# Performance work log

Hardware: AMD Instinct MI355X
Metric: run time of the kernel (lower is better)

Reference implementation:

```python
import jax, jax.numpy as jnp
import numpy as np

H = 16        # heads
DH = 64       # dim_head
DM = 1024     # query_dim = context_dim
INNER = H * DH


def setup_inputs() -> dict:
    key = jax.random.key(0)
    ks = jax.random.split(key, 5)
    s = 0.02
    queries = jax.random.normal(ks[0], (2, 2048, DM), dtype=jnp.float32)
    Wq = jax.random.normal(ks[1], (DM, INNER), dtype=jnp.float32) * s
    Wkv = jax.random.normal(ks[2], (DM, 2 * INNER), dtype=jnp.float32) * s
    Wo = jax.random.normal(ks[3], (INNER, DM), dtype=jnp.float32) * s
    bo = jax.random.normal(ks[4], (DM,), dtype=jnp.float32) * s
    return {"queries": queries, "Wq": Wq, "Wkv": Wkv, "Wo": Wo, "bo": bo}


def reference(queries, Wq, Wkv, Wo, bo):
    b, n, _ = queries.shape
    scale = DH ** -0.5
    q = queries @ Wq                       # [b, n, inner]
    kv = queries @ Wkv                     # self-attention: context = queries
    k, v = jnp.split(kv, 2, axis=-1)
    # b n (h d) -> b h n d
    split_heads = lambda t: t.reshape(b, n, H, DH).transpose(0, 2, 1, 3)
    q, k, v = map(split_heads, (q, k, v))
    sim = jnp.einsum('bhid,bhjd->bhij', q, k) * scale
    attn = jax.nn.softmax(sim, axis=-1)    # dropout is identity (p=0 / eval)
    out = jnp.einsum('bhij,bhjd->bhid', attn, v)
    out = out.transpose(0, 2, 1, 3).reshape(b, n, INNER)
    return out @ Wo + bo
```

## Files before the change

### kernel.cpp

```cpp
#include <hip/hip_runtime.h>
#include <math.h>
#include <stdint.h>

typedef _Float16 half8v __attribute__((ext_vector_type(8)));
typedef _Float16 half4v __attribute__((ext_vector_type(4)));
typedef _Float16 half2v __attribute__((ext_vector_type(2)));
typedef __fp16 fp16x2 __attribute__((ext_vector_type(2)));
typedef float floatx4 __attribute__((ext_vector_type(4)));

#define MFMA16(a, b, c) __builtin_amdgcn_mfma_f32_16x16x32_f16(a, b, c, 0, 0, 0)

#define QSCALE 0.18033688011112f

__device__ __forceinline__ void gld_lds16(const void* g, void* l) {
  __builtin_amdgcn_global_load_lds(
      (const __attribute__((address_space(1))) uint32_t*)(uintptr_t)g,
      (__attribute__((address_space(3))) uint32_t*)(uintptr_t)l, 16, 0, 0);
}

__device__ __forceinline__ half2v pk16(float a, float b) {
  fp16x2 t = __builtin_amdgcn_cvt_pkrtz(a, b);
  return __builtin_bit_cast(half2v, t);
}

__device__ __forceinline__ int swz(int row, int blk) {
  return row * 64 + ((blk ^ (row & 7)) << 3);
}

__device__ __forceinline__ int vswz(int row, int blk) {
  return row * 32 + ((blk ^ ((row >> 1) & 3)) << 3);
}

__device__ __forceinline__ int gswz(int row, int blk) {
  return row * 32 + ((blk ^ ((row >> 1) & 3)) << 3);
}

__global__ __launch_bounds__(256) void prep(
    const float* __restrict__ X, const float* __restrict__ Wq,
    const float* __restrict__ Wkv, const float* __restrict__ Wo,
    _Float16* __restrict__ X16, _Float16* __restrict__ WqkvT,
    _Float16* __restrict__ WoT)
{
  __shared__ alignas(16) _Float16 Tt[64 * 68];
  const int bid = blockIdx.x;
  if (bid < 2048) {
    size_t gid = (size_t)bid * 256 + threadIdx.x;
    const float4* src = (const float4*)(X) + gid * 2;
    float4 a = src[0], b = src[1];
    half8v h;
    h[0]=(_Float16)a.x; h[1]=(_Float16)a.y; h[2]=(_Float16)a.z; h[3]=(_Float16)a.w;
    h[4]=(_Float16)b.x; h[5]=(_Float16)b.y; h[6]=(_Float16)b.z; h[7]=(_Float16)b.w;
    *((half8v*)X16 + gid) = h;
    return;
  }
  int b = bid - 2048;
  const float* src; _Float16* dst; int N, tk, tn;
  if (b < 256)      { src = Wq;  dst = WqkvT;                 N = 1024; tk = b & 15;        tn = b >> 4; }
  else if (b < 768) { src = Wkv; dst = WqkvT + (size_t)1024 * 1024; N = 2048; tk = (b - 256) & 15; tn = (b - 256) >> 4; }
  else              { src = Wo;  dst = WoT;                   N = 1024; tk = (b - 768) & 15; tn = (b - 768) >> 4; }

  const int t = threadIdx.x;
  {
    int kg = t >> 4, ng = t & 15;
    const float* sp = src + (size_t)(tk * 64 + kg * 4) * N + tn * 64 + ng * 4;
    float4 r0 = *(const float4*)(sp);
    float4 r1 = *(const float4*)(sp + N);
    float4 r2 = *(const float4*)(sp + 2 * N);
    float4 r3 = *(const float4*)(sp + 3 * N);
    half4v h;
    h[0]=(_Float16)r0.x; h[1]=(_Float16)r1.x; h[2]=(_Float16)r2.x; h[3]=(_Float16)r3.x;
    *(half4v*)&Tt[(ng * 4 + 0) * 68 + kg * 4] = h;
    h[0]=(_Float16)r0.y; h[1]=(_Float16)r1.y; h[2]=(_Float16)r2.y; h[3]=(_Float16)r3.y;
    *(half4v*)&Tt[(ng * 4 + 1) * 68 + kg * 4] = h;
    h[0]=(_Float16)r0.z; h[1]=(_Float16)r1.z; h[2]=(_Float16)r2.z; h[3]=(_Float16)r3.z;
    *(half4v*)&Tt[(ng * 4 + 2) * 68 + kg * 4] = h;
    h[0]=(_Float16)r0.w; h[1]=(_Float16)r1.w; h[2]=(_Float16)r2.w; h[3]=(_Float16)r3.w;
    *(half4v*)&Tt[(ng * 4 + 3) * 68 + kg * 4] = h;
  }
  __syncthreads();
  #pragma unroll
  for (int i = 0; i < 2; i++) {
    int idx = t + i * 256;
    int nl = idx >> 3, k8 = (idx & 7) * 8;
    half8v v = *(half8v*)&Tt[nl * 68 + k8];
    *(half8v*)(dst + (size_t)(tn * 64 + nl) * 1024 + tk * 64 + k8) = v;
  }
}

__global__ __launch_bounds__(256) void qkv_gemm(
    const _Float16* __restrict__ X16, const _Float16* __restrict__ WqkvT,
    _Float16* __restrict__ q_ws, _Float16* __restrict__ k_ws,
    _Float16* __restrict__ vT_ws)
{
  constexpr int K = 1024;
  __shared__ alignas(16) _Float16 Tt[128 * 136];
  _Float16* As = Tt;
  _Float16* Bs = Tt + 4096;

  const int m0 = blockIdx.x * 128;
  const int n0 = blockIdx.y * 128;

  const int tid  = threadIdx.x;
  const int wave = tid >> 6, lane = tid & 63;
  const int qd = lane >> 4, l15 = lane & 15;
  const int wr = (wave >> 1) * 64, wc = (wave & 1) * 64;
  const int r0i = tid >> 2;
  const int cbs = (((tid & 3) ^ ((r0i >> 1) & 3))) * 8;

  floatx4 acc[4][4] = {};

  for (int k0 = 0; k0 < K; k0 += 32) {
    gld_lds16(X16 + (size_t)(m0 + r0i) * K + k0 + cbs, &As[tid * 8]);
    gld_lds16(X16 + (size_t)(m0 + 64 + r0i) * K + k0 + cbs, &As[(tid + 256) * 8]);
    gld_lds16(WqkvT + (size_t)(n0 + r0i) * K + k0 + cbs, &Bs[tid * 8]);
    gld_lds16(WqkvT + (size_t)(n0 + 64 + r0i) * K + k0 + cbs, &Bs[(tid + 256) * 8]);
    __syncthreads();
    half8v a[4], b[4];
    #pragma unroll
    for (int it = 0; it < 4; it++)
      a[it] = *(half8v*)&As[gswz(wr + it * 16 + l15, qd)];
    #pragma unroll
    for (int jt = 0; jt < 4; jt++)
      b[jt] = *(half8v*)&Bs[gswz(wc + jt * 16 + l15, qd)];
    #pragma unroll
    for (int it = 0; it < 4; it++)
      #pragma unroll
      for (int jt = 0; jt < 4; jt++)
        acc[it][jt] = MFMA16(a[it], b[jt], acc[it][jt]);
    __syncthreads();
  }

  if (n0 < 2048) {
    #pragma unroll
    for (int it = 0; it < 4; it++) {
      #pragma unroll
      for (int jt = 0; jt < 4; jt++) {
        #pragma unroll
        for (int r = 0; r < 4; r++) {
          int m = m0 + wr + it * 16 + qd * 4 + r;
          int n = n0 + wc + jt * 16 + l15;
          float val = acc[it][jt][r];
          int bb = m >> 11, nn = m & 2047;
          if (n0 < 1024) {
            int h = n >> 6, d = n & 63;
            q_ws[(((size_t)bb * 16 + h) * 2048 + nn) * 64 + d] = (_Float16)(val * QSCALE);
          } else {
            int c = n - 1024, h = c >> 6, d = c & 63;
            k_ws[(((size_t)bb * 16 + h) * 2048 + nn) * 64 + d] = (_Float16)val;
          }
        }
      }
    }
  } else {
    #pragma unroll
    for (int it = 0; it < 4; it++) {
      #pragma unroll
      for (int jt = 0; jt < 4; jt++) {
        #pragma unroll
        for (int r = 0; r < 4; r++) {
          int ml = wr + it * 16 + qd * 4 + r;
          int nl = wc + jt * 16 + l15;
          Tt[nl * 136 + ml] = (_Float16)acc[it][jt][r];
        }
      }
    }
    __syncthreads();
    int row = tid >> 1;
    int mh  = (tid & 1) * 64;
    int c   = (n0 - 2048) + row;
    int bb  = m0 >> 11;
    int nnb = (m0 & 2047) + mh;
    _Float16* dstp =
        vT_ws + (((size_t)bb * 16 + (c >> 6)) * 64 + (c & 63)) * 2048 + nnb;
    #pragma unroll
    for (int i = 0; i < 8; i++)
      *(half8v*)(dstp + i * 8) = *(half8v*)&Tt[row * 136 + mh + i * 8];
  }
}

__global__ __launch_bounds__(256, 4) void attn_kernel(
    const _Float16* __restrict__ q_ws, const _Float16* __restrict__ k_ws,
    const _Float16* __restrict__ vT_ws, _Float16* __restrict__ aout)
{
  constexpr int N = 2048;
  __shared__ alignas(16) _Float16 Qs[64 * 64];
  __shared__ alignas(16) _Float16 Ks[2][32 * 64];
  __shared__ alignas(16) _Float16 Vts[2][64 * 32];

  const int id = blockIdx.x;
  const int bh = ((id >> 8) << 3) | (id & 7);
  const int qt = (id >> 3) & 31;

  const _Float16* Qp = q_ws + (size_t)bh * N * 64;
  const _Float16* Kp = k_ws + (size_t)bh * N * 64;
  const _Float16* Vp = vT_ws + (size_t)bh * 64 * N;

  const int tid = threadIdx.x, wave = tid >> 6, lane = tid & 63;
  const int qd = lane >> 4, l15 = lane & 15;
  const int q0 = qt * 64;
  const int wbase = wave * 16;

  #pragma unroll
  for (int i = 0; i < 2; i++) {
    int idx = tid + i * 256;
    int r = idx >> 3, cb = (idx ^ r) & 7;
    gld_lds16(Qp + (size_t)(q0 + r) * 64 + cb * 8, &Qs[idx * 8]);
  }
  { int r = tid >> 3, cb = (tid ^ r) & 7;
    gld_lds16(Kp + (size_t)r * 64 + cb * 8, &Ks[0][tid * 8]); }
  { int r = tid >> 2, cb = ((tid & 3) ^ ((r >> 1) & 3));
    gld_lds16(Vp + (size_t)r * N + cb * 8, &Vts[0][tid * 8]); }
  __syncthreads();

  half8v qf[2];
  #pragma unroll
  for (int ks = 0; ks < 2; ks++)
    qf[ks] = *(half8v*)&Qs[swz(wbase + l15, ks * 4 + qd)];

  floatx4 o[4] = {};
  float lsum = 0.f;

  int p = 0;
  for (int kv0 = 0; kv0 < N; kv0 += 32) {
    const bool more = (kv0 + 32) < N;
    if (more) {
      int kvn = kv0 + 32;
      { int r = tid >> 3, cb = (tid ^ r) & 7;
        gld_lds16(Kp + (size_t)(kvn + r) * 64 + cb * 8, &Ks[p ^ 1][tid * 8]); }
      { int r = tid >> 2, cb = ((tid & 3) ^ ((r >> 1) & 3));
        gld_lds16(Vp + (size_t)r * N + kvn + cb * 8, &Vts[p ^ 1][tid * 8]); }
    }

    floatx4 s[2] = {};
    #pragma unroll
    for (int ks = 0; ks < 2; ks++) {
      half8v kf[2];
      #pragma unroll
      for (int nt = 0; nt < 2; nt++)
        kf[nt] = *(half8v*)&Ks[p][swz(nt * 16 + l15, ks * 4 + qd)];
      #pragma unroll
      for (int nt = 0; nt < 2; nt++)
        s[nt] = MFMA16(kf[nt], qf[ks], s[nt]);
    }

    #pragma unroll
    for (int nt = 0; nt < 2; nt++) {
      float p0 = __builtin_amdgcn_exp2f(s[nt][0]);
      float p1 = __builtin_amdgcn_exp2f(s[nt][1]);
      float p2 = __builtin_amdgcn_exp2f(s[nt][2]);
      float p3 = __builtin_amdgcn_exp2f(s[nt][3]);
      lsum += (p0 + p1) + (p2 + p3);
      half2v h01 = pk16(p0, p1);
      half2v h23 = pk16(p2, p3);
      half4v pk;
      pk[0] = h01[0]; pk[1] = h01[1]; pk[2] = h23[0]; pk[3] = h23[1];
      *(half4v*)&Qs[swz(wbase + l15, 2 * nt + (qd >> 1)) + (qd & 1) * 4] = pk;
    }

    {
      half8v pf = *(half8v*)&Qs[swz(wbase + l15, qd)];
      half8v vf[4];
      #pragma unroll
      for (int dt = 0; dt < 4; dt++)
        vf[dt] = *(half8v*)&Vts[p][vswz(dt * 16 + l15, qd)];
      #pragma unroll
      for (int dt = 0; dt < 4; dt++)
        o[dt] = MFMA16(pf, vf[dt], o[dt]);
    }

    if (more) __syncthreads();
    p ^= 1;
  }

  lsum += __shfl_xor(lsum, 16);
  lsum += __shfl_xor(lsum, 32);

  const int bb = bh >> 4, hh = bh & 15;
  #pragma unroll
  for (int r = 0; r < 4; r++) {
    float inv = 1.0f / __shfl(lsum, qd * 4 + r);
    int n = q0 + wbase + qd * 4 + r;
    #pragma unroll
    for (int dt = 0; dt < 4; dt++) {
      int d = dt * 16 + l15;
      aout[((size_t)(bb * 2048 + n)) * 1024 + hh * 64 + d] =
          (_Float16)(o[dt][r] * inv);
    }
  }
}

__global__ __launch_bounds__(256) void out_gemm(
    const _Float16* __restrict__ A, const _Float16* __restrict__ WoT,
    const float* __restrict__ bo, float* __restrict__ Out)
{
  constexpr int K = 1024;
  __shared__ alignas(16) _Float16 As[64 * 32];
  __shared__ alignas(16) _Float16 Bs[128 * 32];

  const int m0 = blockIdx.x * 64;
  const int n0 = blockIdx.y * 128;
  const int tid = threadIdx.x;
  const int wave = tid >> 6, lane = tid & 63;
  const int qd = lane >> 4, l15 = lane & 15;
  const int wr = (wave >> 1) * 32, wc = (wave & 1) * 64;
  const int r0i = tid >> 2;
  const int cbs = (((tid & 3) ^ ((r0i >> 1) & 3))) * 8;

  floatx4 acc[2][4] = {};

  for (int k0 = 0; k0 < K; k0 += 32) {
    gld_lds16(A + (size_t)(m0 + r0i) * K + k0 + cbs, &As[tid * 8]);
    gld_lds16(WoT + (size_t)(n0 + r0i) * K + k0 + cbs, &Bs[tid * 8]);
    gld_lds16(WoT + (size_t)(n0 + 64 + r0i) * K + k0 + cbs, &Bs[(tid + 256) * 8]);
    __syncthreads();
    half8v a[2], b[4];
    #pragma unroll
    for (int it = 0; it < 2; it++)
      a[it] = *(half8v*)&As[gswz(wr + it * 16 + l15, qd)];
    #pragma unroll
    for (int jt = 0; jt < 4; jt++)
      b[jt] = *(half8v*)&Bs[gswz(wc + jt * 16 + l15, qd)];
    #pragma unroll
    for (int it = 0; it < 2; it++)
      #pragma unroll
      for (int jt = 0; jt < 4; jt++)
        acc[it][jt] = MFMA16(a[it], b[jt], acc[it][jt]);
    __syncthreads();
  }

  #pragma unroll
  for (int it = 0; it < 2; it++) {
    #pragma unroll
    for (int jt = 0; jt < 4; jt++) {
      int n = n0 + wc + jt * 16 + l15;
      float bias = bo[n];
      #pragma unroll
      for (int r = 0; r < 4; r++) {
        int m = m0 + wr + it * 16 + qd * 4 + r;
        Out[(size_t)m * 1024 + n] = acc[it][jt][r] + bias;
      }
    }
  }
}

extern "C" void kernel_launch(void* const* d_in, const int* in_sizes, int n_in,
                              void* d_out, int out_size, void* d_ws, size_t ws_size,
                              hipStream_t stream) {
  const float* X   = (const float*)d_in[0];
  const float* Wq  = (const float*)d_in[1];
  const float* Wkv = (const float*)d_in[2];
  const float* Wo  = (const float*)d_in[3];
  const float* bo  = (const float*)d_in[4];
  float* out = (float*)d_out;

  const size_t M4 = (size_t)4 * 1024 * 1024;
  _Float16* q_ws   = (_Float16*)d_ws;
  _Float16* k_ws   = q_ws + M4;
  _Float16* vT_ws  = k_ws + M4;
  _Float16* X16    = vT_ws + M4;
  _Float16* WqkvT  = X16 + M4;
  _Float16* WoT    = WqkvT + (size_t)3 * 1024 * 1024;
  _Float16* aout   = X16;

  prep<<<3072, 256, 0, stream>>>(X, Wq, Wkv, Wo, X16, WqkvT, WoT);
  qkv_gemm<<<dim3(32, 24), 256, 0, stream>>>(X16, WqkvT, q_ws, k_ws, vT_ws);
  attn_kernel<<<1024, 256, 0, stream>>>(q_ws, k_ws, vT_ws, aout);
  out_gemm<<<dim3(64, 8), 256, 0, stream>>>(aout, WoT, bo, out);
}
```

Before: 186.9 us.

## Deepen K/V prefetch to four LDS buffers with explicit vmcnt waits

The attention kernel's K/V staging grows from a double buffer to a four-slot ring with prefetch distance two. The per-iteration __syncthreads is replaced by explicit s_waitcnt vmcnt counts plus a single s_barrier. s_setprio hints are added around the MFMA sections. The intent is to hide more global-load latency and drop the trailing barrier. In exchange, LDS use roughly doubles, which could lower occupancy at 4 blocks per CU, and the ordering depends on hand-set vmcnt counts.

```diff
diff --git a/kernel.cpp b/kernel.cpp
--- a/kernel.cpp
+++ b/kernel.cpp
@@ -183,9 +183,10 @@
     const _Float16* __restrict__ vT_ws, _Float16* __restrict__ aout)
 {
   constexpr int N = 2048;
+  constexpr int NT = N / 32;
   __shared__ alignas(16) _Float16 Qs[64 * 64];
-  __shared__ alignas(16) _Float16 Ks[2][32 * 64];
-  __shared__ alignas(16) _Float16 Vts[2][64 * 32];
+  __shared__ alignas(16) _Float16 Ks[4][32 * 64];
+  __shared__ alignas(16) _Float16 Vts[4][64 * 32];
 
   const int id = blockIdx.x;
   const int bh = ((id >> 8) << 3) | (id & 7);
@@ -200,17 +201,23 @@
   const int q0 = qt * 64;
   const int wbase = wave * 16;
 
+  const int kr = tid >> 3, kcb = (tid ^ kr) & 7;
+  const int vr = tid >> 2, vcb = ((tid & 3) ^ ((vr >> 1) & 3));
+
   #pragma unroll
   for (int i = 0; i < 2; i++) {
     int idx = tid + i * 256;
     int r = idx >> 3, cb = (idx ^ r) & 7;
     gld_lds16(Qp + (size_t)(q0 + r) * 64 + cb * 8, &Qs[idx * 8]);
   }
-  { int r = tid >> 3, cb = (tid ^ r) & 7;
-    gld_lds16(Kp + (size_t)r * 64 + cb * 8, &Ks[0][tid * 8]); }
-  { int r = tid >> 2, cb = ((tid & 3) ^ ((r >> 1) & 3));
-    gld_lds16(Vp + (size_t)r * N + cb * 8, &Vts[0][tid * 8]); }
-  __syncthreads();
+  gld_lds16(Kp + (size_t)kr * 64 + kcb * 8, &Ks[0][tid * 8]);
+  gld_lds16(Vp + (size_t)vr * N + 0 + vcb * 8, &Vts[0][tid * 8]);
+  gld_lds16(Kp + (size_t)(32 + kr) * 64 + kcb * 8, &Ks[1][tid * 8]);
+  gld_lds16(Vp + (size_t)vr * N + 32 + vcb * 8, &Vts[1][tid * 8]);
+
+  asm volatile("s_waitcnt vmcnt(4)" ::: "memory");
+  __builtin_amdgcn_s_barrier();
+  __builtin_amdgcn_sched_barrier(0);
 
   half8v qf[2];
   #pragma unroll
@@ -220,28 +227,37 @@
   floatx4 o[4] = {};
   float lsum = 0.f;
 
-  int p = 0;
-  for (int kv0 = 0; kv0 < N; kv0 += 32) {
-    const bool more = (kv0 + 32) < N;
-    if (more) {
-      int kvn = kv0 + 32;
-      { int r = tid >> 3, cb = (tid ^ r) & 7;
-        gld_lds16(Kp + (size_t)(kvn + r) * 64 + cb * 8, &Ks[p ^ 1][tid * 8]); }
-      { int r = tid >> 2, cb = ((tid & 3) ^ ((r >> 1) & 3));
-        gld_lds16(Vp + (size_t)r * N + kvn + cb * 8, &Vts[p ^ 1][tid * 8]); }
-    }
+  for (int t = 0; t < NT; ++t) {
+    if (t < NT - 2) {
+      int kvn = (t + 2) * 32;
+      int bn = (t + 2) & 3;
+      gld_lds16(Kp + (size_t)(kvn + kr) * 64 + kcb * 8, &Ks[bn][tid * 8]);
+      gld_lds16(Vp + (size_t)vr * N + kvn + vcb * 8, &Vts[bn][tid * 8]);
+      asm volatile("s_waitcnt vmcnt(4)" ::: "memory");
+    } else if (t == NT - 2) {
+      asm volatile("s_waitcnt vmcnt(2)" ::: "memory");
+    } else {
+      asm volatile("s_waitcnt vmcnt(0)" ::: "memory");
+    }
+    __builtin_amdgcn_s_barrier();
+    __builtin_amdgcn_sched_barrier(0);
+
+    const _Float16* Kb = Ks[t & 3];
+    const _Float16* Vb = Vts[t & 3];
 
     floatx4 s[2] = {};
+    __builtin_amdgcn_s_setprio(1);
     #pragma unroll
     for (int ks = 0; ks < 2; ks++) {
       half8v kf[2];
       #pragma unroll
       for (int nt = 0; nt < 2; nt++)
-        kf[nt] = *(half8v*)&Ks[p][swz(nt * 16 + l15, ks * 4 + qd)];
+        kf[nt] = *(half8v*)&Kb[swz(nt * 16 + l15, ks * 4 + qd)];
       #pragma unroll
       for (int nt = 0; nt < 2; nt++)
         s[nt] = MFMA16(kf[nt], qf[ks], s[nt]);
     }
+    __builtin_amdgcn_s_setprio(0);
 
     #pragma unroll
     for (int nt = 0; nt < 2; nt++) {
@@ -262,14 +278,13 @@
       half8v vf[4];
       #pragma unroll
       for (int dt = 0; dt < 4; dt++)
-        vf[dt] = *(half8v*)&Vts[p][vswz(dt * 16 + l15, qd)];
+        vf[dt] = *(half8v*)&Vb[vswz(dt * 16 + l15, qd)];
+      __builtin_amdgcn_s_setprio(1);
       #pragma unroll
       for (int dt = 0; dt < 4; dt++)
         o[dt] = MFMA16(pf, vf[dt], o[dt]);
-    }
-
-    if (more) __syncthreads();
-    p ^= 1;
+      __builtin_amdgcn_s_setprio(0);
+    }
   }
 
   lsum += __shfl_xor(lsum, 16);
```

Result: no change. 185.6 us (-0.7%).
